# Performance work log

Hardware: AMD Instinct MI355X
Metric: run time of the kernel (lower is better)

Reference implementation:

```python
import jax, jax.numpy as jnp
import numpy as np

NUM_CLUSTERS = 16
HIDDEN = 1024
BOTTLENECK = 128
N_TOKENS = 65536


def setup_inputs() -> dict:
    key = jax.random.key(0)
    k_h, k_ids, k_w1, k_b1, k_w2, k_b2 = jax.random.split(key, 6)
    h = jax.random.normal(k_h, (N_TOKENS, HIDDEN), dtype=jnp.float32)
    cluster_ids = jax.random.randint(k_ids, (N_TOKENS,), 0, NUM_CLUSTERS)
    # Stacked per-cluster adapter params (torch Linear: y = x @ W.T + b; we store
    # already-transposed weights so forward is x @ W1[c]).
    s1 = 1.0 / np.sqrt(HIDDEN)
    s2 = 1.0 / np.sqrt(BOTTLENECK)
    W1 = jax.random.uniform(k_w1, (NUM_CLUSTERS, HIDDEN, BOTTLENECK), jnp.float32, -s1, s1)
    b1 = jax.random.uniform(k_b1, (NUM_CLUSTERS, BOTTLENECK), jnp.float32, -s1, s1)
    # Original inits these to zero; use small random values so grads are non-trivial.
    W2 = jax.random.uniform(k_w2, (NUM_CLUSTERS, BOTTLENECK, HIDDEN), jnp.float32, -s2, s2) * 0.02
    b2 = jax.random.uniform(k_b2, (NUM_CLUSTERS, HIDDEN), jnp.float32, -s2, s2) * 0.02
    return {"h": h, "cluster_ids": cluster_ids, "W1": W1, "b1": b1, "W2": W2, "b2": b2}


def reference(h, cluster_ids, W1, b1, W2, b2):
    # h: [N, H]; cluster_ids: [N]; W1: [K, H, B]; b1: [K, B]; W2: [K, B, H]; b2: [K, H]
    # out[n] = h[n] + adapter_{cluster_ids[n]}(h[n])
    K = W1.shape[0]
    out = jnp.zeros_like(h)
    for c in range(K):  # fixed small expert count; select per-token result via where
        mid = jax.nn.gelu(h @ W1[c] + b1[c], approximate=False)  # [N, B]
        y = h + mid @ W2[c] + b2[c]                               # [N, H]
        out = jnp.where((cluster_ids == c)[:, None], y, out)
    return out
```

## Files before the change

### kernel.cpp

```cpp
#include <hip/hip_runtime.h>
#include <hip/hip_bf16.h>
#include <math.h>

#define NUM_CLUSTERS 16
#define HIDDEN 1024
#define BOT 128
#define NTOK 65536

typedef __attribute__((ext_vector_type(8))) short bf16x8;
typedef __attribute__((ext_vector_type(4))) float f32x4;

typedef __attribute__((address_space(3))) unsigned int lds_u32;
typedef const __attribute__((address_space(1))) unsigned int glb_u32;

__device__ __forceinline__ void gload16(const void* g, void* l) {
  __builtin_amdgcn_global_load_lds((glb_u32*)g, (lds_u32*)l, 16, 0, 0);
}

__device__ __forceinline__ unsigned short f2bf(float x) {
  union { float f; unsigned u; } v; v.f = x;
  unsigned r = v.u + 0x7fffu + ((v.u >> 16) & 1u);
  return (unsigned short)(r >> 16);
}

__device__ __forceinline__ bf16x8 pack8(float4 a, float4 b) {
  bf16x8 r;
  r[0] = (short)f2bf(a.x); r[1] = (short)f2bf(a.y);
  r[2] = (short)f2bf(a.z); r[3] = (short)f2bf(a.w);
  r[4] = (short)f2bf(b.x); r[5] = (short)f2bf(b.y);
  r[6] = (short)f2bf(b.z); r[7] = (short)f2bf(b.w);
  return r;
}

#define SWZS(row, sidx) ((sidx) ^ (((row) & 7) << 3))

#define SCB() __builtin_amdgcn_sched_barrier(0)
#define VMW(n)                                          \
  do {                                                  \
    SCB();                                              \
    asm volatile("s_waitcnt vmcnt(" #n ")" ::: "memory"); \
    SCB();                                              \
  } while (0)
#define SBAR()                                  \
  do {                                          \
    SCB();                                      \
    __builtin_amdgcn_s_barrier();               \
    SCB();                                      \
  } while (0)
#define LGKM0() asm volatile("s_waitcnt lgkmcnt(0)" ::: "memory")

__device__ __forceinline__ int xcd_swz(int bid, int nwg) {
  const int nx = 8;
  int q = nwg / nx, r = nwg % nx;
  int xcd = bid % nx, idx = bid / nx;
  int b = (xcd < r) ? xcd * (q + 1) : r * (q + 1) + (xcd - r) * q;
  return b + idx;
}


__global__ void k_bcnt(const int* __restrict__ ids, int* __restrict__ bcnt) {
  __shared__ int lh[NUM_CLUSTERS];
  const int tid = threadIdx.x, b = blockIdx.x;
  if (tid < NUM_CLUSTERS) lh[tid] = 0;
  __syncthreads();
  atomicAdd(&lh[ids[b * 256 + tid]], 1);
  __syncthreads();
  if (tid < NUM_CLUSTERS) bcnt[tid * 256 + b] = lh[tid];
}

__global__ void k_bscan(const int* __restrict__ bcnt, int* __restrict__ bbase,
                        int* __restrict__ offsets) {
  __shared__ int tot[NUM_CLUSTERS];
  const int tid = threadIdx.x;
  if (tid < NUM_CLUSTERS) {
    int s = 0;
    for (int b = 0; b < 256; ++b) {
      bbase[tid * 256 + b] = s;
      s += bcnt[tid * 256 + b];
    }
    tot[tid] = s;
  }
  __syncthreads();
  if (tid == 0) {
    int s = 0;
    for (int c = 0; c < NUM_CLUSTERS; ++c) { offsets[c] = s; s += tot[c]; }
    offsets[NUM_CLUSTERS] = s;
  }
  __syncthreads();
  if (tid < NUM_CLUSTERS) {
    const int base = offsets[tid];
    for (int b = 0; b < 256; ++b) bbase[tid * 256 + b] += base;
  }
}

__global__ void k_sscat(const int* __restrict__ ids, const int* __restrict__ bbase,
                        int* __restrict__ perm) {
  __shared__ int sIds[256];
  const int tid = threadIdx.x, b = blockIdx.x;
  const int i = b * 256 + tid;
  const int c = ids[i];
  sIds[tid] = c;
  __syncthreads();
  int rank = 0;
  #pragma unroll 8
  for (int j = 0; j < 256; ++j) rank += (j < tid && sIds[j] == c) ? 1 : 0;
  perm[bbase[c * 256 + b] + rank] = i;
}

__global__ void k_w1til(const float* __restrict__ W1, unsigned short* __restrict__ outw) {
  const int id = blockIdx.x * 256 + threadIdx.x;
  const int c  = id >> 14;
  const int ks = (id >> 10) & 15;
  const int q  = id & 1023;
  const int o  = q << 4;
  const int row = o >> 7;
  const int lb  = (o & 127) ^ ((row & 7) << 4);
  const int k0  = ks * 64 + (lb >> 1);
  const float* src = W1 + ((size_t)c * HIDDEN + k0) * BOT + row;
  unsigned short v[8];
  #pragma unroll
  for (int j = 0; j < 8; ++j) v[j] = f2bf(src[(size_t)j * BOT]);
  *(uint4*)((char*)outw + ((size_t)(c * 16 + ks)) * 16384 + o) = *(const uint4*)v;
}

__global__ void k_w2lin(const float* __restrict__ W2, unsigned short* __restrict__ outw) {
  const int id = blockIdx.x * 256 + threadIdx.x;
  const int c   = id >> 14;
  const int rem = id & 16383;
  const int fg  = rem >> 6;
  const int l   = rem & 63;
  const int nc  = fg >> 4, kk = (fg >> 2) & 3, nf = fg & 3;
  const int n   = nc * 64 + nf * 16 + (l & 15);
  const int k0  = kk * 32 + (l >> 4) * 8;
  const float* src = W2 + ((size_t)c * BOT + k0) * HIDDEN + n;
  unsigned short v[8];
  #pragma unroll
  for (int j = 0; j < 8; ++j) v[j] = f2bf(src[(size_t)j * HIDDEN]);
  *(uint4*)(outw + (size_t)id * 8) = *(const uint4*)v;
}

__global__ void k_w2til(const float* __restrict__ W2, unsigned short* __restrict__ outw) {
  const int id = blockIdx.x * 256 + threadIdx.x;
  const int c  = id >> 14;
  const int nc = (id >> 10) & 15;
  const int q  = id & 1023;
  const int o  = q << 4;
  const int row = o >> 8;
  const int lb  = (o & 255) ^ ((row & 7) << 4);
  const int b0  = lb >> 1;
  const int n   = nc * 64 + row;
  const float* src = W2 + ((size_t)c * BOT + b0) * HIDDEN + n;
  unsigned short v[8];
  #pragma unroll
  for (int j = 0; j < 8; ++j) v[j] = f2bf(src[(size_t)j * HIDDEN]);
  *(uint4*)((char*)outw + ((size_t)(c * 16 + nc)) * 16384 + o) = *(const uint4*)v;
}

__device__ __forceinline__ bool locate(const int* offsets, int bid, int TMv,
                                       int& c, int& base, int& nvalid) {
  int t = bid;
  for (c = 0; c < NUM_CLUSTERS; ++c) {
    int cnt = offsets[c + 1] - offsets[c];
    int nt = (cnt + TMv - 1) / TMv;
    if (t < nt) {
      base = offsets[c] + t * TMv;
      nvalid = min(TMv, offsets[c + 1] - base);
      return true;
    }
    t -= nt;
  }
  return false;
}

__global__ __launch_bounds__(512, 6) void k_fuse(
    const float* __restrict__ h, const float* __restrict__ b1g,
    const float* __restrict__ b2g, const unsigned short* __restrict__ W1til,
    const unsigned short* __restrict__ W2lin, const int* __restrict__ offsets,
    const int* __restrict__ perm, float* __restrict__ out) {

  __shared__ __align__(16) unsigned short sA[2][4096];
  __shared__ __align__(16) unsigned short sB[2][8192];
  __shared__ int sTok[64];

  const int tid = threadIdx.x;
  const int l = tid & 63, w = tid >> 6;
  const int lr = l & 15, lg = l >> 4;
  const int wr = w >> 2, wc = w & 3;
  const int row = tid >> 3, o8 = tid & 7;

  const int nwg = NTOK / 64 + NUM_CLUSTERS;
  int c, base, nvalid;
  if (!locate(offsets, xcd_swz(blockIdx.x, nwg), 64, c, base, nvalid)) return;

  if (tid < 64) sTok[tid] = perm[base + min(tid, nvalid - 1)];
  LGKM0();
  SBAR();

  const unsigned short* w1base = W1til + (size_t)c * 16 * 8192;
  const unsigned short* wlin   = W2lin + (size_t)c * 131072;
  const float* hrow = h + (long)sTok[row] * HIDDEN + o8 * 8;

  float4 vaA[2], vaB[2];
  vaA[0] = *(const float4*)(hrow);       vaA[1] = *(const float4*)(hrow + 4);
  SCB();
  gload16(w1base + tid * 8, &sB[0][tid * 8]);
  gload16(w1base + 4096 + tid * 8, &sB[0][4096 + tid * 8]);
  SCB();
  vaB[0] = *(const float4*)(hrow + 64);  vaB[1] = *(const float4*)(hrow + 68);
  SCB();
  *(bf16x8*)&sA[0][SWZS(row, row * 64 + o8 * 8)] = pack8(vaA[0], vaA[1]);
  LGKM0();
  VMW(2);
  SBAR();

  f32x4 acc[2][2];
  #pragma unroll
  for (int i = 0; i < 2; ++i)
    #pragma unroll
    for (int j = 0; j < 2; ++j) { f32x4 z = {0.f, 0.f, 0.f, 0.f}; acc[i][j] = z; }

#define G1_MFMA(CUR)                                                          \
  do {                                                                        \
    _Pragma("unroll")                                                         \
    for (int kk = 0; kk < 2; ++kk) {                                          \
      bf16x8 af[2], bfr[2];                                                   \
      _Pragma("unroll")                                                       \
      for (int mf = 0; mf < 2; ++mf) {                                        \
        const int m = wr * 32 + mf * 16 + lr;                                 \
        af[mf] = *(const bf16x8*)&sA[CUR][SWZS(m, m * 64 + kk * 32 + lg * 8)];\
      }                                                                       \
      _Pragma("unroll")                                                       \
      for (int nf = 0; nf < 2; ++nf) {                                        \
        const int rn = wc * 32 + nf * 16 + lr;                                \
        bfr[nf] = *(const bf16x8*)&sB[CUR][SWZS(rn, rn * 64 + kk * 32 + lg * 8)]; \
      }                                                                       \
      _Pragma("unroll")                                                       \
      for (int mf = 0; mf < 2; ++mf)                                          \
        _Pragma("unroll")                                                     \
        for (int nf = 0; nf < 2; ++nf)                                        \
          acc[mf][nf] = __builtin_amdgcn_mfma_f32_16x16x32_bf16(              \
              af[mf], bfr[nf], acc[mf][nf], 0, 0, 0);                         \
    }                                                                         \
  } while (0)

  #pragma unroll
  for (int t = 0; t < 16; ++t) {
    const int cur = t & 1;
    if (t < 15) {
      const unsigned short* w1s = w1base + (t + 1) * 8192;
      gload16(w1s + tid * 8, &sB[cur ^ 1][tid * 8]);
      gload16(w1s + 4096 + tid * 8, &sB[cur ^ 1][4096 + tid * 8]);
      SCB();
    }
    if (t < 14) {
      if (t & 1) {
        vaB[0] = *(const float4*)(hrow + (t + 2) * 64);
        vaB[1] = *(const float4*)(hrow + (t + 2) * 64 + 4);
      } else {
        vaA[0] = *(const float4*)(hrow + (t + 2) * 64);
        vaA[1] = *(const float4*)(hrow + (t + 2) * 64 + 4);
      }
      SCB();
    }
    G1_MFMA(cur);
    if (t < 15) {
      const float4* src = ((t + 1) & 1) ? vaB : vaA;
      *(bf16x8*)&sA[cur ^ 1][SWZS(row, row * 64 + o8 * 8)] = pack8(src[0], src[1]);
      if (t < 14) { VMW(2); } else { VMW(0); }
      LGKM0();
      SBAR();
    }
  }
#undef G1_MFMA

  unsigned short* sMid = &sA[0][0];
  gload16(wlin + tid * 8, &sB[0][tid * 8]);
  gload16(wlin + 4096 + tid * 8, &sB[0][4096 + tid * 8]);
  SCB();
  SBAR();

  {
    float b1v[2];
    #pragma unroll
    for (int nf = 0; nf < 2; ++nf) b1v[nf] = b1g[c * BOT + wc * 32 + nf * 16 + lr];
    #pragma unroll
    for (int mf = 0; mf < 2; ++mf) {
      #pragma unroll
      for (int nf = 0; nf < 2; ++nf) {
        #pragma unroll
        for (int r = 0; r < 4; ++r) {
          float x = acc[mf][nf][r] + b1v[nf];
          float g = 0.5f * x * (1.0f + erff(x * 0.70710678118654752f));
          const int m = wr * 32 + mf * 16 + lg * 4 + r;
          const int n = wc * 32 + nf * 16 + lr;
          sMid[SWZS(m, m * 128 + n)] = f2bf(g);
        }
      }
    }
  }
  LGKM0();
  VMW(0);
  SBAR();

  const int wrow = (w & 3) * 16;
  const int ch = w >> 2;

  bf16x8 ma[4];
  {
    const int mrow = wrow + lr;
    #pragma unroll
    for (int kk = 0; kk < 4; ++kk)
      ma[kk] = *(const bf16x8*)&sMid[SWZS(mrow, mrow * 128 + kk * 32 + lg * 8)];
  }

  const float* hr[4];
  float* orp[4];
  #pragma unroll
  for (int r = 0; r < 4; ++r) {
    const long tk = (long)sTok[wrow + lg * 4 + r] * HIDDEN;
    hr[r] = h + tk;
    orp[r] = out + tk;
  }
  const float* b2c = b2g + c * HIDDEN;

  for (int nc = 0; nc < 16; ++nc) {
    const int cur = nc & 1;
    const int cb = nc * 64 + ch * 32;
    float hv[2][4], bv[2];
    #pragma unroll
    for (int nf = 0; nf < 2; ++nf)
      #pragma unroll
      for (int r = 0; r < 4; ++r)
        hv[nf][r] = hr[r][cb + nf * 16 + lr];
    #pragma unroll
    for (int nf = 0; nf < 2; ++nf) bv[nf] = b2c[cb + nf * 16 + lr];
    SCB();
    if (nc < 15) {
      const unsigned short* ws2 = wlin + (nc + 1) * 8192;
      gload16(ws2 + tid * 8, &sB[cur ^ 1][tid * 8]);
      gload16(ws2 + 4096 + tid * 8, &sB[cur ^ 1][4096 + tid * 8]);
      SCB();
    }

    f32x4 a2[2];
    { f32x4 z = {0.f, 0.f, 0.f, 0.f}; a2[0] = z; a2[1] = z; }
    #pragma unroll
    for (int kk = 0; kk < 4; ++kk) {
      #pragma unroll
      for (int nf = 0; nf < 2; ++nf) {
        const bf16x8 bf =
            *(const bf16x8*)&sB[cur][(kk * 4 + ch * 2 + nf) * 512 + l * 8];
        a2[nf] = __builtin_amdgcn_mfma_f32_16x16x32_bf16(ma[kk], bf, a2[nf], 0, 0, 0);
      }
    }

    #pragma unroll
    for (int nf = 0; nf < 2; ++nf) {
      #pragma unroll
      for (int r = 0; r < 4; ++r) {
        orp[r][cb + nf * 16 + lr] = a2[nf][r] + hv[nf][r] + bv[nf];
      }
    }
    if (nc < 15) {
      VMW(8);
      SBAR();
    }
  }
}

#define FSWZ(row, sidx) ((sidx) ^ (((row) & 7) << 3))

__global__ __launch_bounds__(256, 2) void k_fused(
    const float* __restrict__ h, const float* __restrict__ b1g,
    const float* __restrict__ b2g, const unsigned short* __restrict__ W1til,
    const unsigned short* __restrict__ W2til, const int* __restrict__ offsets,
    const int* __restrict__ perm, float* __restrict__ out) {

  __shared__ __align__(16) unsigned short sAB[16384];
  __shared__ __align__(16) unsigned short sMid[16384];
  __shared__ int sTok[128];

  const int tid = threadIdx.x;
  const int l = tid & 63, w = tid >> 6;
  const int wr = w >> 1, wc = w & 1;
  const int lr = l & 15, lg = l >> 4;

  int c, base, nvalid;
  if (!locate(offsets, blockIdx.x, 128, c, base, nvalid)) return;

  if (tid < 128) sTok[tid] = perm[base + min(tid, nvalid - 1)];
  __syncthreads();

  const unsigned short* w1base = W1til + (size_t)c * 16 * 8192;
  const unsigned short* w2base = W2til + (size_t)c * 16 * 8192;

  const int arow = tid >> 1, ahalf = tid & 1;
  const long htok = (long)sTok[arow] * HIDDEN;

  f32x4 acc[4][4];
  #pragma unroll
  for (int i = 0; i < 4; ++i)
    #pragma unroll
    for (int j = 0; j < 4; ++j) { f32x4 z = {0.f, 0.f, 0.f, 0.f}; acc[i][j] = z; }

  for (int ks = 0; ks < 16; ++ks) {
    __syncthreads();
    const unsigned short* w1s = w1base + ks * 8192;
    #pragma unroll
    for (int j = 0; j < 4; ++j)
      gload16(w1s + j * 2048 + tid * 8, &sAB[8192 + j * 2048 + tid * 8]);
    {
      const float* hp = h + htok + ks * 64 + ahalf * 32;
      float4 v0 = *(const float4*)(hp + 0),  v1 = *(const float4*)(hp + 4);
      float4 v2 = *(const float4*)(hp + 8),  v3 = *(const float4*)(hp + 12);
      float4 v4 = *(const float4*)(hp + 16), v5 = *(const float4*)(hp + 20);
      float4 v6 = *(const float4*)(hp + 24), v7 = *(const float4*)(hp + 28);
      const int sb = arow * 64 + ahalf * 32;
      *(bf16x8*)&sAB[FSWZ(arow, sb + 0)]  = pack8(v0, v1);
      *(bf16x8*)&sAB[FSWZ(arow, sb + 8)]  = pack8(v2, v3);
      *(bf16x8*)&sAB[FSWZ(arow, sb + 16)] = pack8(v4, v5);
      *(bf16x8*)&sAB[FSWZ(arow, sb + 24)] = pack8(v6, v7);
    }
    __syncthreads();
    #pragma unroll
    for (int kk = 0; kk < 2; ++kk) {
      bf16x8 af[4], bfr[4];
      #pragma unroll
      for (int mf = 0; mf < 4; ++mf) {
        const int rw = wr * 64 + mf * 16 + lr;
        af[mf] = *(const bf16x8*)&sAB[FSWZ(rw, rw * 64 + kk * 32 + lg * 8)];
      }
      #pragma unroll
      for (int nf = 0; nf < 4; ++nf) {
        const int rn = wc * 64 + nf * 16 + lr;
        bfr[nf] = *(const bf16x8*)&sAB[8192 + FSWZ(rn, rn * 64 + kk * 32 + lg * 8)];
      }
      #pragma unroll
      for (int mf = 0; mf < 4; ++mf)
        #pragma unroll
        for (int nf = 0; nf < 4; ++nf)
          acc[mf][nf] = __builtin_amdgcn_mfma_f32_16x16x32_bf16(af[mf], bfr[nf], acc[mf][nf], 0, 0, 0);
    }
  }

  float b1v[4];
  #pragma unroll
  for (int nf = 0; nf < 4; ++nf) b1v[nf] = b1g[c * BOT + wc * 64 + nf * 16 + lr];
  #pragma unroll
  for (int mf = 0; mf < 4; ++mf)
    #pragma unroll
    for (int nf = 0; nf < 4; ++nf)
      #pragma unroll
      for (int r = 0; r < 4; ++r) {
        float x = acc[mf][nf][r] + b1v[nf];
        float g = 0.5f * x * (1.0f + erff(x * 0.70710678118654752f));
        const int m = wr * 64 + mf * 16 + lg * 4 + r;
        const int n = wc * 64 + nf * 16 + lr;
        sMid[FSWZ(m, m * 128 + n)] = f2bf(g);
      }

  for (int nc = 0; nc < 16; ++nc) {
    __syncthreads();
    #pragma unroll
    for (int j = 0; j < 4; ++j)
      gload16(w2base + nc * 8192 + j * 2048 + tid * 8, &sAB[j * 2048 + tid * 8]);
    __syncthreads();

    f32x4 a2[4][2];
    #pragma unroll
    for (int i = 0; i < 4; ++i)
      #pragma unroll
      for (int j = 0; j < 2; ++j) { f32x4 z = {0.f, 0.f, 0.f, 0.f}; a2[i][j] = z; }

    #pragma unroll
    for (int kk = 0; kk < 4; ++kk) {
      bf16x8 af[4], bfr[2];
      #pragma unroll
      for (int mf = 0; mf < 4; ++mf) {
        const int m = wr * 64 + mf * 16 + lr;
        af[mf] = *(const bf16x8*)&sMid[FSWZ(m, m * 128 + kk * 32 + lg * 8)];
      }
      #pragma unroll
      for (int nf = 0; nf < 2; ++nf) {
        const int rn = wc * 32 + nf * 16 + lr;
        bfr[nf] = *(const bf16x8*)&sAB[FSWZ(rn, rn * 128 + kk * 32 + lg * 8)];
      }
      #pragma unroll
      for (int mf = 0; mf < 4; ++mf)
        #pragma unroll
        for (int nf = 0; nf < 2; ++nf)
          a2[mf][nf] = __builtin_amdgcn_mfma_f32_16x16x32_bf16(af[mf], bfr[nf], a2[mf][nf], 0, 0, 0);
    }

    #pragma unroll
    for (int nf = 0; nf < 2; ++nf) {
      const int nn = nc * 64 + wc * 32 + nf * 16 + lr;
      const float b2v = b2g[c * HIDDEN + nn];
      #pragma unroll
      for (int mf = 0; mf < 4; ++mf)
        #pragma unroll
        for (int r = 0; r < 4; ++r) {
          const int m = wr * 64 + mf * 16 + lg * 4 + r;
          if (m < nvalid) {
            const long tk = (long)sTok[m] * HIDDEN;
            out[tk + nn] = h[tk + nn] + a2[mf][nf][r] + b2v;
          }
        }
    }
  }
}

extern "C" void kernel_launch(void* const* d_in, const int* in_sizes, int n_in,
                              void* d_out, int out_size, void* d_ws, size_t ws_size,
                              hipStream_t stream) {
  const float* h   = (const float*)d_in[0];
  const int*   ids = (const int*)d_in[1];
  const float* W1  = (const float*)d_in[2];
  const float* b1  = (const float*)d_in[3];
  const float* W2  = (const float*)d_in[4];
  const float* b2  = (const float*)d_in[5];
  float* out = (float*)d_out;

  char* ws = (char*)d_ws;
  int* offsets = (int*)(ws + 128);
  int* perm    = (int*)(ws + 256);
  int* bcnt    = (int*)(ws + 262400);
  int* bbase   = (int*)(ws + 262400 + 16384);
  unsigned short* W1buf = (unsigned short*)(ws + 262400 + 32768);
  unsigned short* W2buf = W1buf + (size_t)16 * 16 * 8192;
  const size_t need = 262400 + 32768 + 2 * (size_t)16 * 16 * 8192 * 2;

  k_bcnt<<<256, 256, 0, stream>>>(ids, bcnt);
  k_bscan<<<1, 64, 0, stream>>>(bcnt, bbase, offsets);
  k_sscat<<<256, 256, 0, stream>>>(ids, bbase, perm);
  k_w1til<<<1024, 256, 0, stream>>>(W1, W1buf);

  if (ws_size >= need) {
    k_w2lin<<<1024, 256, 0, stream>>>(W2, W2buf);
    const int nwg = NTOK / 64 + NUM_CLUSTERS;
    k_fuse<<<nwg, 512, 0, stream>>>(h, b1, b2, W1buf, W2buf, offsets, perm, out);
  } else {
    k_w2til<<<1024, 256, 0, stream>>>(W2, W2buf);
    k_fused<<<NTOK / 128 + NUM_CLUSTERS, 256, 0, stream>>>(
        h, b1, b2, W1buf, W2buf, offsets, perm, out);
  }
}
```

Measured before the change: 253.5 us.

## Load W1 B-fragments directly into registers in MFMA layout, bypassing LDS

Adds a pre-pass that writes W1 as bf16 in per-lane MFMA fragment order, so the first GEMM loop loads B operands straight from global memory into registers with two-stage register double buffering. This removes the LDS staging, the LDS reads for B and the vmcnt waits for W1 tiles in the GEMM1 loop. In exchange it uses more VGPRs for the prefetch buffers, which could hurt occupancy under the 6-wave launch bound, and exposes global-load latency directly to the MFMA loop.

```diff
diff --git a/kernel.cpp b/kernel.cpp
--- a/kernel.cpp
+++ b/kernel.cpp
@@ -107,6 +107,39 @@
   perm[bbase[c * 256 + b] + rank] = i;
 }
 
+__global__ void k_w1lin(const float* __restrict__ W1, unsigned short* __restrict__ outw) {
+  const int id = blockIdx.x * 256 + threadIdx.x;
+  const int c   = id >> 14;
+  const int rem = id & 16383;
+  const int t   = rem >> 10;
+  const int f   = (rem >> 6) & 15;
+  const int l   = rem & 63;
+  const int wc = f >> 2, kk = (f >> 1) & 1, nf = f & 1;
+  const int rn = wc * 32 + nf * 16 + (l & 15);
+  const int k0 = t * 64 + kk * 32 + (l >> 4) * 8;
+  const float* src = W1 + ((size_t)c * HIDDEN + k0) * BOT + rn;
+  unsigned short v[8];
+  #pragma unroll
+  for (int j = 0; j < 8; ++j) v[j] = f2bf(src[(size_t)j * BOT]);
+  *(uint4*)(outw + (size_t)id * 8) = *(const uint4*)v;
+}
+
+__global__ void k_w2lin(const float* __restrict__ W2, unsigned short* __restrict__ outw) {
+  const int id = blockIdx.x * 256 + threadIdx.x;
+  const int c   = id >> 14;
+  const int rem = id & 16383;
+  const int fg  = rem >> 6;
+  const int l   = rem & 63;
+  const int nc  = fg >> 4, kk = (fg >> 2) & 3, nf = fg & 3;
+  const int n   = nc * 64 + nf * 16 + (l & 15);
+  const int k0  = kk * 32 + (l >> 4) * 8;
+  const float* src = W2 + ((size_t)c * BOT + k0) * HIDDEN + n;
+  unsigned short v[8];
+  #pragma unroll
+  for (int j = 0; j < 8; ++j) v[j] = f2bf(src[(size_t)j * HIDDEN]);
+  *(uint4*)(outw + (size_t)id * 8) = *(const uint4*)v;
+}
+
 __global__ void k_w1til(const float* __restrict__ W1, unsigned short* __restrict__ outw) {
   const int id = blockIdx.x * 256 + threadIdx.x;
   const int c  = id >> 14;
@@ -121,22 +154,6 @@
   #pragma unroll
   for (int j = 0; j < 8; ++j) v[j] = f2bf(src[(size_t)j * BOT]);
   *(uint4*)((char*)outw + ((size_t)(c * 16 + ks)) * 16384 + o) = *(const uint4*)v;
-}
-
-__global__ void k_w2lin(const float* __restrict__ W2, unsigned short* __restrict__ outw) {
-  const int id = blockIdx.x * 256 + threadIdx.x;
-  const int c   = id >> 14;
-  const int rem = id & 16383;
-  const int fg  = rem >> 6;
-  const int l   = rem & 63;
-  const int nc  = fg >> 4, kk = (fg >> 2) & 3, nf = fg & 3;
-  const int n   = nc * 64 + nf * 16 + (l & 15);
-  const int k0  = kk * 32 + (l >> 4) * 8;
-  const float* src = W2 + ((size_t)c * BOT + k0) * HIDDEN + n;
-  unsigned short v[8];
-  #pragma unroll
-  for (int j = 0; j < 8; ++j) v[j] = f2bf(src[(size_t)j * HIDDEN]);
-  *(uint4*)(outw + (size_t)id * 8) = *(const uint4*)v;
 }
 
 __global__ void k_w2til(const float* __restrict__ W2, unsigned short* __restrict__ outw) {
@@ -172,9 +189,10 @@
   return false;
 }
 
+
 __global__ __launch_bounds__(512, 6) void k_fuse(
     const float* __restrict__ h, const float* __restrict__ b1g,
-    const float* __restrict__ b2g, const unsigned short* __restrict__ W1til,
+    const float* __restrict__ b2g, const unsigned short* __restrict__ W1lin,
     const unsigned short* __restrict__ W2lin, const int* __restrict__ offsets,
     const int* __restrict__ perm, float* __restrict__ out) {
 
@@ -196,21 +214,28 @@
   LGKM0();
   SBAR();
 
-  const unsigned short* w1base = W1til + (size_t)c * 16 * 8192;
-  const unsigned short* wlin   = W2lin + (size_t)c * 131072;
+  const unsigned short* wfrag = W1lin + (size_t)c * 131072 + (wc * 4) * 512 + l * 8;
+  const unsigned short* wlin  = W2lin + (size_t)c * 131072;
   const float* hrow = h + (long)sTok[row] * HIDDEN + o8 * 8;
+
+  bf16x8 rBA[4], rBB[4];
+#define LOADF(DST, T)                                                  \
+  do {                                                                 \
+    _Pragma("unroll")                                                  \
+    for (int j = 0; j < 4; ++j)                                        \
+      DST[j] = *(const bf16x8*)(wfrag + (T) * 8192 + j * 512);         \
+    SCB();                                                             \
+  } while (0)
 
   float4 vaA[2], vaB[2];
   vaA[0] = *(const float4*)(hrow);       vaA[1] = *(const float4*)(hrow + 4);
   SCB();
-  gload16(w1base + tid * 8, &sB[0][tid * 8]);
-  gload16(w1base + 4096 + tid * 8, &sB[0][4096 + tid * 8]);
-  SCB();
+  LOADF(rBA, 0);
   vaB[0] = *(const float4*)(hrow + 64);  vaB[1] = *(const float4*)(hrow + 68);
   SCB();
+  LOADF(rBB, 1);
   *(bf16x8*)&sA[0][SWZS(row, row * 64 + o8 * 8)] = pack8(vaA[0], vaA[1]);
   LGKM0();
-  VMW(2);
   SBAR();
 
   f32x4 acc[2][2];
@@ -219,39 +244,28 @@
     #pragma unroll
     for (int j = 0; j < 2; ++j) { f32x4 z = {0.f, 0.f, 0.f, 0.f}; acc[i][j] = z; }
 
-#define G1_MFMA(CUR)                                                          \
+#define G1_MFMA(CUR, RB)                                                      \
   do {                                                                        \
     _Pragma("unroll")                                                         \
     for (int kk = 0; kk < 2; ++kk) {                                          \
-      bf16x8 af[2], bfr[2];                                                   \
+      bf16x8 af[2];                                                           \
       _Pragma("unroll")                                                       \
       for (int mf = 0; mf < 2; ++mf) {                                        \
         const int m = wr * 32 + mf * 16 + lr;                                 \
         af[mf] = *(const bf16x8*)&sA[CUR][SWZS(m, m * 64 + kk * 32 + lg * 8)];\
       }                                                                       \
       _Pragma("unroll")                                                       \
-      for (int nf = 0; nf < 2; ++nf) {                                        \
-        const int rn = wc * 32 + nf * 16 + lr;                                \
-        bfr[nf] = *(const bf16x8*)&sB[CUR][SWZS(rn, rn * 64 + kk * 32 + lg * 8)]; \
-      }                                                                       \
-      _Pragma("unroll")                                                       \
       for (int mf = 0; mf < 2; ++mf)                                          \
         _Pragma("unroll")                                                     \
         for (int nf = 0; nf < 2; ++nf)                                        \
           acc[mf][nf] = __builtin_amdgcn_mfma_f32_16x16x32_bf16(              \
-              af[mf], bfr[nf], acc[mf][nf], 0, 0, 0);                         \
+              af[mf], RB[kk * 2 + nf], acc[mf][nf], 0, 0, 0);                 \
     }                                                                         \
   } while (0)
 
   #pragma unroll
   for (int t = 0; t < 16; ++t) {
     const int cur = t & 1;
-    if (t < 15) {
-      const unsigned short* w1s = w1base + (t + 1) * 8192;
-      gload16(w1s + tid * 8, &sB[cur ^ 1][tid * 8]);
-      gload16(w1s + 4096 + tid * 8, &sB[cur ^ 1][4096 + tid * 8]);
-      SCB();
-    }
     if (t < 14) {
       if (t & 1) {
         vaB[0] = *(const float4*)(hrow + (t + 2) * 64);
@@ -262,16 +276,19 @@
       }
       SCB();
     }
-    G1_MFMA(cur);
+    if (cur == 0) { G1_MFMA(0, rBA); } else { G1_MFMA(1, rBB); }
+    if (t < 14) {
+      if (cur == 0) { LOADF(rBA, t + 2); } else { LOADF(rBB, t + 2); }
+    }
     if (t < 15) {
       const float4* src = ((t + 1) & 1) ? vaB : vaA;
       *(bf16x8*)&sA[cur ^ 1][SWZS(row, row * 64 + o8 * 8)] = pack8(src[0], src[1]);
-      if (t < 14) { VMW(2); } else { VMW(0); }
       LGKM0();
       SBAR();
     }
   }
 #undef G1_MFMA
+#undef LOADF
 
   unsigned short* sMid = &sA[0][0];
   gload16(wlin + tid * 8, &sB[0][tid * 8]);
@@ -533,13 +550,14 @@
   k_bcnt<<<256, 256, 0, stream>>>(ids, bcnt);
   k_bscan<<<1, 64, 0, stream>>>(bcnt, bbase, offsets);
   k_sscat<<<256, 256, 0, stream>>>(ids, bbase, perm);
-  k_w1til<<<1024, 256, 0, stream>>>(W1, W1buf);
 
   if (ws_size >= need) {
+    k_w1lin<<<1024, 256, 0, stream>>>(W1, W1buf);
     k_w2lin<<<1024, 256, 0, stream>>>(W2, W2buf);
     const int nwg = NTOK / 64 + NUM_CLUSTERS;
     k_fuse<<<nwg, 512, 0, stream>>>(h, b1, b2, W1buf, W2buf, offsets, perm, out);
   } else {
+    k_w1til<<<1024, 256, 0, stream>>>(W1, W1buf);
     k_w2til<<<1024, 256, 0, stream>>>(W2, W2buf);
     k_fused<<<NTOK / 128 + NUM_CLUSTERS, 256, 0, stream>>>(
         h, b1, b2, W1buf, W2buf, offsets, perm, out);
```

After: 249.8 us. Within noise of the previous version (-1.5%).
